# Optimization experiments

Measured on AMD Instinct MI355X. Metric: run time of the kernel, lower is better.

Reference implementation:

```python
import jax, jax.numpy as jnp
import numpy as np

NUM_HEADS, HEAD_SIZE = 8, 80
C = NUM_HEADS * HEAD_SIZE  # 640
GROUPS = 32
EPS = 1e-5


def group_norm(x, gamma, beta):
    b, h, w, c = x.shape
    xg = x.reshape(b, h, w, GROUPS, c // GROUPS)
    mean = xg.mean(axis=(1, 2, 4), keepdims=True)
    var = xg.var(axis=(1, 2, 4), keepdims=True)
    xg = (xg - mean) * jax.lax.rsqrt(var + EPS)
    return xg.reshape(b, h, w, c) * gamma + beta


def layer_norm(x, gamma, beta):
    mean = x.mean(axis=-1, keepdims=True)
    var = x.var(axis=-1, keepdims=True)
    return (x - mean) * jax.lax.rsqrt(var + EPS) * gamma + beta


def cross_attention(x, ctx, wq, wk, wv, wo, bo):
    # x: [B,S,C], ctx: [B,T,Cc]
    b, s, _ = x.shape
    t = ctx.shape[1]
    q = (x @ wq).reshape(b, s, NUM_HEADS, HEAD_SIZE)
    k = (ctx @ wk).reshape(b, t, NUM_HEADS, HEAD_SIZE)
    v = (ctx @ wv).reshape(b, t, NUM_HEADS, HEAD_SIZE)
    scale = HEAD_SIZE ** -0.5
    score = jnp.einsum('bqnh,bknh->bnqk', q, k) * scale
    weights = jax.nn.softmax(score, axis=-1)
    attn = jnp.einsum('bnqk,bknh->bqnh', weights, v)
    return attn.reshape(b, s, C) @ wo + bo


def geglu(x, w, b):
    p = x @ w + b
    xh, gate = p[..., :2560], p[..., 2560:]
    tanh_res = jnp.tanh(gate * 0.7978845608 * (1.0 + 0.044715 * gate * gate))
    return xh * 0.5 * gate * (1.0 + tanh_res)


def setup_inputs() -> dict:
    key = jax.random.key(0)
    ks = iter(jax.random.split(key, 32))
    rn = lambda shape, s=0.02: jax.random.normal(next(ks), shape, dtype=jnp.float32) * s
    inp = {
        'x': jax.random.normal(next(ks), (8, 32, 32, 640), dtype=jnp.float32),
        'context': jax.random.normal(next(ks), (8, 77, 768), dtype=jnp.float32),
        'gn_gamma': jnp.ones((640,), jnp.float32), 'gn_beta': jnp.zeros((640,), jnp.float32),
        'proj_in_w': rn((640, 640)), 'proj_in_b': jnp.zeros((640,), jnp.float32),
        'ln1_g': jnp.ones((640,), jnp.float32), 'ln1_b': jnp.zeros((640,), jnp.float32),
        'a1_q': rn((640, 640)), 'a1_k': rn((640, 640)), 'a1_v': rn((640, 640)),
        'a1_o': rn((640, 640)), 'a1_ob': jnp.zeros((640,), jnp.float32),
        'ln2_g': jnp.ones((640,), jnp.float32), 'ln2_b': jnp.zeros((640,), jnp.float32),
        'a2_q': rn((640, 640)), 'a2_k': rn((768, 640)), 'a2_v': rn((768, 640)),
        'a2_o': rn((640, 640)), 'a2_ob': jnp.zeros((640,), jnp.float32),
        'ln3_g': jnp.ones((640,), jnp.float32), 'ln3_b': jnp.zeros((640,), jnp.float32),
        'ff1_w': rn((640, 5120)), 'ff1_b': jnp.zeros((5120,), jnp.float32),
        'ff2_w': rn((2560, 640)), 'ff2_b': jnp.zeros((640,), jnp.float32),
        'proj_out_w': rn((640, 640)), 'proj_out_b': jnp.zeros((640,), jnp.float32),
    }
    return inp


def reference(x, context, gn_gamma, gn_beta, proj_in_w, proj_in_b,
              ln1_g, ln1_b, a1_q, a1_k, a1_v, a1_o, a1_ob,
              ln2_g, ln2_b, a2_q, a2_k, a2_v, a2_o, a2_ob,
              ln3_g, ln3_b, ff1_w, ff1_b, ff2_w, ff2_b,
              proj_out_w, proj_out_b):
    b, h, w, c = x.shape
    # GroupNorm + 1x1 conv proj_in (== dense over channels)
    y = group_norm(x, gn_gamma, gn_beta)
    y = y @ proj_in_w + proj_in_b
    y = y.reshape(b, h * w, c)
    # Transformer block
    t = cross_attention(layer_norm(y, ln1_g, ln1_b), layer_norm(y, ln1_g, ln1_b), a1_q, a1_k, a1_v, a1_o, a1_ob) + y
    t = cross_attention(layer_norm(t, ln2_g, ln2_b), context, a2_q, a2_k, a2_v, a2_o, a2_ob) + t
    t = geglu(layer_norm(t, ln3_g, ln3_b), ff1_w, ff1_b) @ ff2_w + ff2_b + t
    # proj_out (1x1 conv) + residual
    t = t.reshape(b, h, w, c)
    return t @ proj_out_w + proj_out_b + x
```

## Files before the change

kernel.cpp:

```cpp
#include <hip/hip_runtime.h>
#include <hip/hip_bf16.h>
#include <math.h>

typedef unsigned short u16;
typedef unsigned int u32;
typedef __attribute__((ext_vector_type(8))) short bf16x8;
typedef __attribute__((ext_vector_type(4))) float f32x4;

__device__ __forceinline__ u16 f2b(float f) {
    union { float f; unsigned u; } v; v.f = f;
    unsigned r = v.u + 0x7fffu + ((v.u >> 16) & 1u);
    return (u16)(r >> 16);
}
__device__ __forceinline__ float b2f(u16 h) {
    union { unsigned u; float f; } v; v.u = ((unsigned)h) << 16; return v.f;
}

__device__ __forceinline__ void gld16(const u16* gp, u16* lp) {
    auto g = (const __attribute__((address_space(1))) u32*)gp;
    auto l = (__attribute__((address_space(3))) u32*)lp;
    __builtin_amdgcn_global_load_lds(g, l, 16, 0, 0);
}

__device__ __forceinline__ int swz8(int row, int lb) { return (lb + (row >> 1)) & 7; }

struct GemmP {
    const u16* A; const float* Af; const u16* B;
    const float* bias; const float* res;
    float* Cf; u16* Cb;
    int M, N, K, lda, ldb, ldc;
    float alpha;
};

template<int MT>
__global__ __launch_bounds__(256) void gemm_bt(GemmP p) {
    constexpr int MI = MT / 32;
    __shared__ u16 As[MT * 64];
    __shared__ u16 Bs[128 * 64];
    const int tid = threadIdx.x;
    const int m0 = blockIdx.y * MT, n0 = blockIdx.x * 128;
    const int lane = tid & 63, wave = tid >> 6;
    const int quad = lane >> 4, l16 = lane & 15;
    const int wr = (wave >> 1) * (MT / 2), wc = (wave & 1) * 64;
    const int srow = lane >> 3, pb8 = lane & 7;

    f32x4 acc[MI][4];
#pragma unroll
    for (int i = 0; i < MI; i++)
#pragma unroll
        for (int j = 0; j < 4; j++) acc[i][j] = (f32x4){0.f, 0.f, 0.f, 0.f};

    for (int k0 = 0; k0 < p.K; k0 += 64) {
        if (p.Af) {
            constexpr int TPR = 256 / MT;
            constexpr int NB = 8 / TPR;
            int row = tid / TPR, part = tid % TPR;
            const float* srcr = p.Af + (long)(m0 + row) * p.lda + k0;
#pragma unroll
            for (int q2 = 0; q2 < NB; q2++) {
                int lb = part * NB + q2;
                float4 f0 = *(const float4*)(srcr + lb * 8);
                float4 f1 = *(const float4*)(srcr + lb * 8 + 4);
                u16 tmp[8];
                tmp[0]=f2b(f0.x); tmp[1]=f2b(f0.y); tmp[2]=f2b(f0.z); tmp[3]=f2b(f0.w);
                tmp[4]=f2b(f1.x); tmp[5]=f2b(f1.y); tmp[6]=f2b(f1.z); tmp[7]=f2b(f1.w);
                *(uint4*)&As[row * 64 + swz8(row, lb) * 8] = *(uint4*)tmp;
            }
        } else {
#pragma unroll
            for (int j = 0; j < MT / 32; j++) {
                int rbase = wave * (MT / 4) + j * 8;
                int r = rbase + srow;
                int lb = (pb8 - (r >> 1)) & 7;
                gld16(p.A + (long)(m0 + r) * p.lda + k0 + lb * 8, &As[rbase * 64]);
            }
        }
#pragma unroll
        for (int j = 0; j < 4; j++) {
            int rbase = wave * 32 + j * 8;
            int r = rbase + srow;
            int lb = (pb8 - (r >> 1)) & 7;
            gld16(p.B + (long)(n0 + r) * p.ldb + k0 + lb * 8, &Bs[rbase * 64]);
        }
        __syncthreads();

#pragma unroll
        for (int kk = 0; kk < 2; kk++) {
            bf16x8 af[MI], bfr[4];
#pragma unroll
            for (int mi = 0; mi < MI; mi++) {
                int row = wr + mi * 16 + l16;
                af[mi] = *(const bf16x8*)&As[row * 64 + swz8(row, kk * 4 + quad) * 8];
            }
#pragma unroll
            for (int ni = 0; ni < 4; ni++) {
                int row = wc + ni * 16 + l16;
                bfr[ni] = *(const bf16x8*)&Bs[row * 64 + swz8(row, kk * 4 + quad) * 8];
            }
#pragma unroll
            for (int mi = 0; mi < MI; mi++)
#pragma unroll
                for (int ni = 0; ni < 4; ni++)
                    acc[mi][ni] = __builtin_amdgcn_mfma_f32_16x16x32_bf16(af[mi], bfr[ni], acc[mi][ni], 0, 0, 0);
        }
        __syncthreads();
    }

#pragma unroll
    for (int mi = 0; mi < MI; mi++) {
#pragma unroll
        for (int ni = 0; ni < 4; ni++) {
#pragma unroll
            for (int r = 0; r < 4; r++) {
                int row = m0 + wr + mi * 16 + quad * 4 + r;
                int col = n0 + wc + ni * 16 + l16;
                if (row < p.M && col < p.N) {
                    float v = acc[mi][ni][r] * p.alpha;
                    if (p.bias) v += p.bias[col];
                    long idx = (long)row * p.ldc + col;
                    if (p.res) v += p.res[idx];
                    if (p.Cf) p.Cf[idx] = v; else p.Cb[idx] = f2b(v);
                }
            }
        }
    }
}

struct GegluP {
    const u16* A; const u16* Bx; const u16* Bg;
    const float* bx; const float* bg;
    u16* H;
    int K, lda, ldb, ldh;
};

__global__ __launch_bounds__(256) void gemm_geglu(GegluP p) {
    __shared__ u16 As[128 * 64];
    __shared__ u16 Bxs[128 * 64];
    __shared__ u16 Bgs[128 * 64];
    const int tid = threadIdx.x;
    const int m0 = blockIdx.y * 128, n0 = blockIdx.x * 128;
    const int lane = tid & 63, wave = tid >> 6;
    const int quad = lane >> 4, l16 = lane & 15;
    const int wr = (wave >> 1) * 64, wc = (wave & 1) * 64;
    const int srow = lane >> 3, pb8 = lane & 7;

    f32x4 ax[4][4], ag[4][4];
#pragma unroll
    for (int i = 0; i < 4; i++)
#pragma unroll
        for (int j = 0; j < 4; j++) { ax[i][j] = (f32x4){0.f,0.f,0.f,0.f}; ag[i][j] = (f32x4){0.f,0.f,0.f,0.f}; }

    for (int k0 = 0; k0 < p.K; k0 += 64) {
#pragma unroll
        for (int j = 0; j < 4; j++) {
            int rbase = wave * 32 + j * 8;
            int r = rbase + srow;
            int lb = (pb8 - (r >> 1)) & 7;
            gld16(p.A  + (long)(m0 + r) * p.lda + k0 + lb * 8, &As[rbase * 64]);
            gld16(p.Bx + (long)(n0 + r) * p.ldb + k0 + lb * 8, &Bxs[rbase * 64]);
            gld16(p.Bg + (long)(n0 + r) * p.ldb + k0 + lb * 8, &Bgs[rbase * 64]);
        }
        __syncthreads();

#pragma unroll
        for (int kk = 0; kk < 2; kk++) {
            bf16x8 af[4], bxf[4], bgf[4];
#pragma unroll
            for (int mi = 0; mi < 4; mi++) {
                int row = wr + mi * 16 + l16;
                af[mi] = *(const bf16x8*)&As[row * 64 + swz8(row, kk * 4 + quad) * 8];
            }
#pragma unroll
            for (int ni = 0; ni < 4; ni++) {
                int row = wc + ni * 16 + l16;
                bxf[ni] = *(const bf16x8*)&Bxs[row * 64 + swz8(row, kk * 4 + quad) * 8];
                bgf[ni] = *(const bf16x8*)&Bgs[row * 64 + swz8(row, kk * 4 + quad) * 8];
            }
#pragma unroll
            for (int mi = 0; mi < 4; mi++)
#pragma unroll
                for (int ni = 0; ni < 4; ni++) {
                    ax[mi][ni] = __builtin_amdgcn_mfma_f32_16x16x32_bf16(af[mi], bxf[ni], ax[mi][ni], 0, 0, 0);
                    ag[mi][ni] = __builtin_amdgcn_mfma_f32_16x16x32_bf16(af[mi], bgf[ni], ag[mi][ni], 0, 0, 0);
                }
        }
        __syncthreads();
    }

#pragma unroll
    for (int mi = 0; mi < 4; mi++) {
#pragma unroll
        for (int ni = 0; ni < 4; ni++) {
#pragma unroll
            for (int r = 0; r < 4; r++) {
                int row = m0 + wr + mi * 16 + quad * 4 + r;
                int col = wc + ni * 16 + l16;
                float xh = ax[mi][ni][r] + p.bx[n0 + col];
                float g  = ag[mi][ni][r] + p.bg[n0 + col];
                float u  = 0.7978845608f * g * (1.0f + 0.044715f * g * g);
                float s  = 1.0f / (1.0f + __expf(-2.0f * u));
                p.H[(long)row * p.ldh + n0 + col] = f2b(xh * g * s);
            }
        }
    }
}

struct FlashP {
    const u16* Q; const u16* K; const u16* V;
    u16* O;
    int ldq, ldk, ldv, ldo;
    int S, TS, nIter;
    long qBatch, kBatch;
    float scale;
};

__global__ __launch_bounds__(256, 2) void flash_attn(FlashP p) {
    __shared__ u16 shU[128 * 136];
    __shared__ u16 shV[80 * 136];
    const int z = blockIdx.x, b = z >> 3, h = z & 7;
    const int q0 = blockIdx.z * 128;
    const int tid = threadIdx.x, lane = tid & 63, w = tid >> 6;
    const int quad = lane >> 4, l16 = lane & 15;

    const u16* Qp = p.Q + (long)b * p.qBatch + (long)q0 * p.ldq + h * 80;
    const u16* Kp = p.K + (long)b * p.kBatch + h * 80;
    const u16* Vp = p.V + (long)b * p.kBatch + h * 80;

    for (int idx = tid; idx < 128 * 12; idx += 256) {
        int row = idx / 12, g = idx - row * 12;
        uint4 v = {0, 0, 0, 0};
        if (g < 10) v = *(const uint4*)(Qp + (long)row * p.ldq + g * 8);
        *(uint4*)&shU[row * 104 + g * 8] = v;
    }
    __syncthreads();
    bf16x8 qf[2][3];
#pragma unroll
    for (int mi = 0; mi < 2; mi++)
#pragma unroll
        for (int kk = 0; kk < 3; kk++)
            qf[mi][kk] = *(const bf16x8*)&shU[(w * 32 + mi * 16 + l16) * 104 + kk * 32 + quad * 8];
    __syncthreads();

    float m_[2][4], l_[2][4];
    f32x4 acc_o[2][5];
#pragma unroll
    for (int mi = 0; mi < 2; mi++) {
#pragma unroll
        for (int r = 0; r < 4; r++) { m_[mi][r] = -1e30f; l_[mi][r] = 0.f; }
#pragma unroll
        for (int ni = 0; ni < 5; ni++) acc_o[mi][ni] = (f32x4){0.f, 0.f, 0.f, 0.f};
    }

    for (int it = 0; it < p.nIter; it++) {
        const int s0 = it * 128;
        for (int idx = tid; idx < 128 * 12; idx += 256) {
            int row = idx / 12, g = idx - row * 12;
            uint4 v = {0, 0, 0, 0};
            if (g < 10 && (s0 + row) < p.TS)
                v = *(const uint4*)(Kp + (long)(s0 + row) * p.ldk + g * 8);
            *(uint4*)&shU[row * 104 + g * 8] = v;
        }
        for (int idx = tid; idx < 128 * 10; idx += 256) {
            int row = idx / 10, g = idx - row * 10;
            uint4 v = {0, 0, 0, 0};
            if ((s0 + row) < p.TS)
                v = *(const uint4*)(Vp + (long)(s0 + row) * p.ldv + g * 8);
            u16 tmp[8]; *(uint4*)tmp = v;
#pragma unroll
            for (int j = 0; j < 8; j++) shV[(g * 8 + j) * 136 + row] = tmp[j];
        }
        __syncthreads();

        f32x4 acc_s[2][8];
#pragma unroll
        for (int mi = 0; mi < 2; mi++)
#pragma unroll
            for (int ni = 0; ni < 8; ni++) acc_s[mi][ni] = (f32x4){0.f, 0.f, 0.f, 0.f};
#pragma unroll
        for (int kk = 0; kk < 3; kk++) {
            bf16x8 kf[8];
#pragma unroll
            for (int ni = 0; ni < 8; ni++)
                kf[ni] = *(const bf16x8*)&shU[(ni * 16 + l16) * 104 + kk * 32 + quad * 8];
#pragma unroll
            for (int mi = 0; mi < 2; mi++)
#pragma unroll
                for (int ni = 0; ni < 8; ni++)
                    acc_s[mi][ni] = __builtin_amdgcn_mfma_f32_16x16x32_bf16(qf[mi][kk], kf[ni], acc_s[mi][ni], 0, 0, 0);
        }
        __syncthreads();

#pragma unroll
        for (int mi = 0; mi < 2; mi++) {
#pragma unroll
            for (int ni = 0; ni < 8; ni++) {
                bool valid = (s0 + ni * 16 + l16) < p.TS;
#pragma unroll
                for (int r = 0; r < 4; r++)
                    acc_s[mi][ni][r] = valid ? acc_s[mi][ni][r] * p.scale : -1e30f;
            }
#pragma unroll
            for (int r = 0; r < 4; r++) {
                float rm = acc_s[mi][0][r];
#pragma unroll
                for (int ni = 1; ni < 8; ni++) rm = fmaxf(rm, acc_s[mi][ni][r]);
#pragma unroll
                for (int msk = 1; msk < 16; msk <<= 1) rm = fmaxf(rm, __shfl_xor(rm, msk));
                float mn = fmaxf(m_[mi][r], rm);
                float al = __expf(m_[mi][r] - mn);
                m_[mi][r] = mn;
                float rs = 0.f;
                int prow = (w * 32 + mi * 16 + quad * 4 + r) * 136;
#pragma unroll
                for (int ni = 0; ni < 8; ni++) {
                    float pv = __expf(acc_s[mi][ni][r] - mn);
                    rs += pv;
                    shU[prow + ni * 16 + l16] = f2b(pv);
                }
#pragma unroll
                for (int msk = 1; msk < 16; msk <<= 1) rs += __shfl_xor(rs, msk);
                l_[mi][r] = l_[mi][r] * al + rs;
#pragma unroll
                for (int ni = 0; ni < 5; ni++) acc_o[mi][ni][r] *= al;
            }
        }
        __syncthreads();

#pragma unroll
        for (int kk = 0; kk < 4; kk++) {
            bf16x8 vf[5], pf[2];
#pragma unroll
            for (int ni = 0; ni < 5; ni++)
                vf[ni] = *(const bf16x8*)&shV[(ni * 16 + l16) * 136 + kk * 32 + quad * 8];
#pragma unroll
            for (int mi = 0; mi < 2; mi++)
                pf[mi] = *(const bf16x8*)&shU[(w * 32 + mi * 16 + l16) * 136 + kk * 32 + quad * 8];
#pragma unroll
            for (int mi = 0; mi < 2; mi++)
#pragma unroll
                for (int ni = 0; ni < 5; ni++)
                    acc_o[mi][ni] = __builtin_amdgcn_mfma_f32_16x16x32_bf16(pf[mi], vf[ni], acc_o[mi][ni], 0, 0, 0);
        }
        __syncthreads();
    }

    u16* Op = p.O + ((long)b * p.S + q0) * p.ldo + h * 80;
#pragma unroll
    for (int mi = 0; mi < 2; mi++) {
#pragma unroll
        for (int r = 0; r < 4; r++) {
            float inv = 1.0f / l_[mi][r];
            int row = w * 32 + mi * 16 + quad * 4 + r;
#pragma unroll
            for (int ni = 0; ni < 5; ni++)
                Op[(long)row * p.ldo + ni * 16 + l16] = f2b(acc_o[mi][ni][r] * inv);
        }
    }
}

struct WT8 { const float* W[8]; u16* Wt[8]; };

__global__ void wtrans8(WT8 p, int K, int N) {
    __shared__ float tile[32][33];
    const float* W = p.W[blockIdx.z];
    u16* Wt = p.Wt[blockIdx.z];
    int n0 = blockIdx.x * 32, k0 = blockIdx.y * 32;
    int tx = threadIdx.x, ty = threadIdx.y;
#pragma unroll
    for (int i = 0; i < 4; i++) {
        int k = k0 + ty + i * 8, n = n0 + tx;
        if (k < K && n < N) tile[ty + i * 8][tx] = W[(long)k * N + n];
    }
    __syncthreads();
#pragma unroll
    for (int i = 0; i < 4; i++) {
        int n = n0 + ty + i * 8, k = k0 + tx;
        if (n < N && k < K) Wt[(long)n * K + k] = f2b(tile[tx][ty + i * 8]);
    }
}

__global__ void gn_stats(const float* __restrict__ x, float* __restrict__ stats) {
    int bid = blockIdx.x;
    int b = bid >> 5, g = bid & 31;
    const float* base = x + (long)b * 32 * 32 * 640 + g * 20;
    float s = 0.f, sq = 0.f;
    for (int idx = threadIdx.x; idx < 32 * 32 * 20; idx += 256) {
        int hw = idx / 20, c = idx - hw * 20;
        float v = base[(long)hw * 640 + c];
        s += v; sq += v * v;
    }
    __shared__ float rs[256], rq[256];
    rs[threadIdx.x] = s; rq[threadIdx.x] = sq; __syncthreads();
    for (int t = 128; t > 0; t >>= 1) {
        if (threadIdx.x < t) { rs[threadIdx.x] += rs[threadIdx.x + t]; rq[threadIdx.x] += rq[threadIdx.x + t]; }
        __syncthreads();
    }
    if (threadIdx.x == 0) {
        float mean = rs[0] / 20480.0f;
        float var = rq[0] / 20480.0f - mean * mean;
        stats[bid * 2] = mean;
        stats[bid * 2 + 1] = rsqrtf(var + 1e-5f);
    }
}

__global__ void gn_apply(const float* __restrict__ x, const float* __restrict__ stats,
                         const float* __restrict__ gamma, const float* __restrict__ beta,
                         u16* __restrict__ out) {
    long i = (long)blockIdx.x * 256 + threadIdx.x;
    int c = (int)(i % 640);
    int b = (int)(i / (32 * 32 * 640));
    int g = c / 20;
    float mean = stats[(b * 32 + g) * 2], inv = stats[(b * 32 + g) * 2 + 1];
    out[i] = f2b((x[i] - mean) * inv * gamma[c] + beta[c]);
}

__global__ void layernorm_rows(const float* __restrict__ X, const float* __restrict__ g,
                               const float* __restrict__ be, u16* __restrict__ out, int nrows) {
    int row = blockIdx.x * 4 + (threadIdx.x >> 6);
    int lane = threadIdx.x & 63;
    if (row >= nrows) return;
    const float* x = X + (long)row * 640;
    float v[10];
    float s = 0.f;
#pragma unroll
    for (int i = 0; i < 10; i++) { v[i] = x[lane + i * 64]; s += v[i]; }
#pragma unroll
    for (int m = 1; m < 64; m <<= 1) s += __shfl_xor(s, m);
    float mean = s * (1.0f / 640.0f);
    float sq = 0.f;
#pragma unroll
    for (int i = 0; i < 10; i++) { float d = v[i] - mean; sq += d * d; }
#pragma unroll
    for (int m = 1; m < 64; m <<= 1) sq += __shfl_xor(sq, m);
    float inv = rsqrtf(sq * (1.0f / 640.0f) + 1e-5f);
    u16* o = out + (long)row * 640;
#pragma unroll
    for (int i = 0; i < 10; i++) {
        int c = lane + i * 64;
        o[c] = f2b((v[i] - mean) * inv * g[c] + be[c]);
    }
}

__global__ void f2b_k(const float* __restrict__ src, u16* __restrict__ dst, long n) {
    long i = (long)blockIdx.x * 256 + threadIdx.x;
    if (i < n) dst[i] = f2b(src[i]);
}

extern "C" void kernel_launch(void* const* d_in, const int* in_sizes, int n_in,
                              void* d_out, int out_size, void* d_ws, size_t ws_size,
                              hipStream_t stream) {
    const float* x        = (const float*)d_in[0];
    const float* context  = (const float*)d_in[1];
    const float* gn_gamma = (const float*)d_in[2];
    const float* gn_beta  = (const float*)d_in[3];
    const float* proj_in_w = (const float*)d_in[4];
    const float* proj_in_b = (const float*)d_in[5];
    const float* ln1_g = (const float*)d_in[6];
    const float* ln1_b = (const float*)d_in[7];
    const float* a1_q = (const float*)d_in[8];
    const float* a1_k = (const float*)d_in[9];
    const float* a1_v = (const float*)d_in[10];
    const float* a1_o = (const float*)d_in[11];
    const float* a1_ob = (const float*)d_in[12];
    const float* ln2_g = (const float*)d_in[13];
    const float* ln2_b = (const float*)d_in[14];
    const float* a2_q = (const float*)d_in[15];
    const float* a2_k = (const float*)d_in[16];
    const float* a2_v = (const float*)d_in[17];
    const float* a2_o = (const float*)d_in[18];
    const float* a2_ob = (const float*)d_in[19];
    const float* ln3_g = (const float*)d_in[20];
    const float* ln3_b = (const float*)d_in[21];
    const float* ff1_w = (const float*)d_in[22];
    const float* ff1_b = (const float*)d_in[23];
    const float* ff2_w = (const float*)d_in[24];
    const float* ff2_b = (const float*)d_in[25];
    const float* proj_out_w = (const float*)d_in[26];
    const float* proj_out_b = (const float*)d_in[27];
    float* out = (float*)d_out;

    char* ws = (char*)d_ws;
    size_t off = 0;
    auto alloc = [&](size_t bytes) -> void* {
        void* p = ws + off;
        off += (bytes + 255) & ~(size_t)255;
        return p;
    };
    u16* Wt_pi  = (u16*)alloc(640 * 640 * 2);
    u16* Wt_qkv = (u16*)alloc((size_t)1920 * 640 * 2);
    u16* Wt_1o  = (u16*)alloc(640 * 640 * 2);
    u16* Wt_2q  = (u16*)alloc(640 * 640 * 2);
    u16* Wt_kv2 = (u16*)alloc((size_t)1280 * 768 * 2);
    u16* Wt_2o  = (u16*)alloc(640 * 640 * 2);
    u16* Wt_f1  = (u16*)alloc((size_t)5120 * 640 * 2);
    u16* Wt_f2  = (u16*)alloc((size_t)640 * 2560 * 2);
    u16* Wt_po  = (u16*)alloc(640 * 640 * 2);
    float* t    = (float*)alloc((size_t)8192 * 640 * 4);
    u16* bufA   = (u16*)alloc((size_t)8192 * 640 * 2);
    u16* big    = (u16*)alloc((size_t)8192 * 2560 * 2);
    u16* kv2b   = (u16*)alloc((size_t)616 * 1280 * 2);
    u16* ctxb   = (u16*)alloc((size_t)616 * 768 * 2);
    float* stats = (float*)alloc(256 * 2 * 4);
    (void)alloc(65536);
    u16* qkvb = big;
    u16* hb   = big;

    const float SCALE = 0.11180339887498949f;

    auto gemm1 = [&](const u16* A, const float* Af, const u16* Bt, const float* bias,
                     const float* res, float* Cf, u16* Cb, int M, int N, int K,
                     int lda, int ldb, int ldc, float alpha, int mt) {
        GemmP p{};
        p.A = A; p.Af = Af; p.B = Bt; p.bias = bias; p.res = res; p.Cf = Cf; p.Cb = Cb;
        p.M = M; p.N = N; p.K = K; p.lda = lda; p.ldb = ldb; p.ldc = ldc;
        p.alpha = alpha;
        dim3 grid((N + 127) / 128, (M + mt - 1) / mt, 1);
        if (mt == 64) gemm_bt<64><<<grid, 256, 0, stream>>>(p);
        else          gemm_bt<128><<<grid, 256, 0, stream>>>(p);
    };

    {
        dim3 blk(32, 8);
        WT8 sq{};
        sq.W[0] = proj_in_w; sq.Wt[0] = Wt_pi;
        sq.W[1] = a1_q;      sq.Wt[1] = Wt_qkv;
        sq.W[2] = a1_k;      sq.Wt[2] = Wt_qkv + 640 * 640;
        sq.W[3] = a1_v;      sq.Wt[3] = Wt_qkv + 2 * 640 * 640;
        sq.W[4] = a1_o;      sq.Wt[4] = Wt_1o;
        sq.W[5] = a2_q;      sq.Wt[5] = Wt_2q;
        sq.W[6] = a2_o;      sq.Wt[6] = Wt_2o;
        sq.W[7] = proj_out_w; sq.Wt[7] = Wt_po;
        wtrans8<<<dim3(20, 20, 8), blk, 0, stream>>>(sq, 640, 640);
        WT8 kv{};
        kv.W[0] = a2_k; kv.Wt[0] = Wt_kv2;
        kv.W[1] = a2_v; kv.Wt[1] = Wt_kv2 + (size_t)640 * 768;
        wtrans8<<<dim3(20, 24, 2), blk, 0, stream>>>(kv, 768, 640);
        WT8 f1{}; f1.W[0] = ff1_w; f1.Wt[0] = Wt_f1;
        wtrans8<<<dim3(160, 20, 1), blk, 0, stream>>>(f1, 640, 5120);
        WT8 f2{}; f2.W[0] = ff2_w; f2.Wt[0] = Wt_f2;
        wtrans8<<<dim3(20, 80, 1), blk, 0, stream>>>(f2, 2560, 640);
    }

    gn_stats<<<256, 256, 0, stream>>>(x, stats);
    gn_apply<<<20480, 256, 0, stream>>>(x, stats, gn_gamma, gn_beta, bufA);
    gemm1(bufA, nullptr, Wt_pi, proj_in_b, nullptr, t, nullptr, 8192, 640, 640, 640, 640, 640, 1.0f, 64);

    layernorm_rows<<<2048, 256, 0, stream>>>(t, ln1_g, ln1_b, bufA, 8192);
    gemm1(bufA, nullptr, Wt_qkv, nullptr, nullptr, nullptr, qkvb, 8192, 1920, 640, 640, 640, 1920, 1.0f, 128);
    {
        FlashP p{};
        p.Q = qkvb; p.K = qkvb + 640; p.V = qkvb + 1280; p.O = bufA;
        p.ldq = 1920; p.ldk = 1920; p.ldv = 1920; p.ldo = 640;
        p.S = 1024; p.TS = 1024; p.nIter = 8;
        p.qBatch = (long)1024 * 1920; p.kBatch = (long)1024 * 1920;
        p.scale = SCALE;
        flash_attn<<<dim3(64, 1, 8), 256, 0, stream>>>(p);
    }
    gemm1(bufA, nullptr, Wt_1o, a1_ob, t, t, nullptr, 8192, 640, 640, 640, 640, 640, 1.0f, 64);

    layernorm_rows<<<2048, 256, 0, stream>>>(t, ln2_g, ln2_b, bufA, 8192);
    f2b_k<<<1848, 256, 0, stream>>>(context, ctxb, 473088);
    gemm1(bufA, nullptr, Wt_2q, nullptr, nullptr, nullptr, qkvb, 8192, 640, 640, 640, 640, 640, 1.0f, 64);
    gemm1(ctxb, nullptr, Wt_kv2, nullptr, nullptr, nullptr, kv2b, 616, 1280, 768, 768, 768, 1280, 1.0f, 64);
    {
        FlashP p{};
        p.Q = qkvb; p.K = kv2b; p.V = kv2b + 640; p.O = bufA;
        p.ldq = 640; p.ldk = 1280; p.ldv = 1280; p.ldo = 640;
        p.S = 1024; p.TS = 77; p.nIter = 1;
        p.qBatch = (long)1024 * 640; p.kBatch = (long)77 * 1280;
        p.scale = SCALE;
        flash_attn<<<dim3(64, 1, 8), 256, 0, stream>>>(p);
    }
    gemm1(bufA, nullptr, Wt_2o, a2_ob, t, t, nullptr, 8192, 640, 640, 640, 640, 640, 1.0f, 64);

    layernorm_rows<<<2048, 256, 0, stream>>>(t, ln3_g, ln3_b, bufA, 8192);
    {
        GegluP p{};
        p.A = bufA; p.Bx = Wt_f1; p.Bg = Wt_f1 + (size_t)2560 * 640;
        p.bx = ff1_b; p.bg = ff1_b + 2560;
        p.H = hb;
        p.K = 640; p.lda = 640; p.ldb = 640; p.ldh = 2560;
        gemm_geglu<<<dim3(20, 64), 256, 0, stream>>>(p);
    }
    gemm1(hb, nullptr, Wt_f2, ff2_b, t, t, nullptr, 8192, 640, 2560, 2560, 2560, 640, 1.0f, 64);

    gemm1(nullptr, t, Wt_po, proj_out_b, x, out, nullptr, 8192, 640, 640, 640, 640, 640, 1.0f, 64);
}
```

Baseline: 699.7 us.

## Double-buffer LDS in GEMM kernels and drop fp32-A load path

```diff
diff --git a/kernel.cpp b/kernel.cpp
--- a/kernel.cpp
+++ b/kernel.cpp
@@ -22,10 +22,10 @@
     __builtin_amdgcn_global_load_lds(g, l, 16, 0, 0);
 }
 
-__device__ __forceinline__ int swz8(int row, int lb) { return (lb + (row >> 1)) & 7; }
+__device__ __forceinline__ int swz4(int row, int q) { return (q + (row >> 1)) & 3; }
 
 struct GemmP {
-    const u16* A; const float* Af; const u16* B;
+    const u16* A; const u16* B;
     const float* bias; const float* res;
     float* Cf; u16* Cb;
     int M, N, K, lda, ldb, ldc;
@@ -35,14 +35,14 @@
 template<int MT>
 __global__ __launch_bounds__(256) void gemm_bt(GemmP p) {
     constexpr int MI = MT / 32;
-    __shared__ u16 As[MT * 64];
-    __shared__ u16 Bs[128 * 64];
+    __shared__ u16 As[2][MT * 64];
+    __shared__ u16 Bs[2][128 * 64];
     const int tid = threadIdx.x;
     const int m0 = blockIdx.y * MT, n0 = blockIdx.x * 128;
     const int lane = tid & 63, wave = tid >> 6;
     const int quad = lane >> 4, l16 = lane & 15;
     const int wr = (wave >> 1) * (MT / 2), wc = (wave & 1) * 64;
-    const int srow = lane >> 3, pb8 = lane & 7;
+    const int srow4 = lane >> 2, pcb4 = lane & 3;
 
     f32x4 acc[MI][4];
 #pragma unroll
@@ -50,52 +50,45 @@
 #pragma unroll
         for (int j = 0; j < 4; j++) acc[i][j] = (f32x4){0.f, 0.f, 0.f, 0.f};
 
-    for (int k0 = 0; k0 < p.K; k0 += 64) {
-        if (p.Af) {
-            constexpr int TPR = 256 / MT;
-            constexpr int NB = 8 / TPR;
-            int row = tid / TPR, part = tid % TPR;
-            const float* srcr = p.Af + (long)(m0 + row) * p.lda + k0;
-#pragma unroll
-            for (int q2 = 0; q2 < NB; q2++) {
-                int lb = part * NB + q2;
-                float4 f0 = *(const float4*)(srcr + lb * 8);
-                float4 f1 = *(const float4*)(srcr + lb * 8 + 4);
-                u16 tmp[8];
-                tmp[0]=f2b(f0.x); tmp[1]=f2b(f0.y); tmp[2]=f2b(f0.z); tmp[3]=f2b(f0.w);
-                tmp[4]=f2b(f1.x); tmp[5]=f2b(f1.y); tmp[6]=f2b(f1.z); tmp[7]=f2b(f1.w);
-                *(uint4*)&As[row * 64 + swz8(row, lb) * 8] = *(uint4*)tmp;
-            }
-        } else {
-#pragma unroll
-            for (int j = 0; j < MT / 32; j++) {
-                int rbase = wave * (MT / 4) + j * 8;
-                int r = rbase + srow;
-                int lb = (pb8 - (r >> 1)) & 7;
-                gld16(p.A + (long)(m0 + r) * p.lda + k0 + lb * 8, &As[rbase * 64]);
-            }
-        }
-#pragma unroll
-        for (int j = 0; j < 4; j++) {
-            int rbase = wave * 32 + j * 8;
-            int r = rbase + srow;
-            int lb = (pb8 - (r >> 1)) & 7;
-            gld16(p.B + (long)(n0 + r) * p.ldb + k0 + lb * 8, &Bs[rbase * 64]);
-        }
-        __syncthreads();
-
-#pragma unroll
-        for (int kk = 0; kk < 2; kk++) {
+    auto stage = [&](int buf, int k0) {
+#pragma unroll
+        for (int c = 0; c < MT / 32; c++) {
+            int cc = wave * (MT / 32) + c;
+            int sub = cc / (MT / 16), rg = cc % (MT / 16);
+            int r = rg * 16 + srow4;
+            int lcb = (pcb4 - (r >> 1)) & 3;
+            gld16(p.A + (long)(m0 + r) * p.lda + k0 + sub * 32 + lcb * 8,
+                  &As[buf][sub * (MT * 32) + rg * 512]);
+        }
+#pragma unroll
+        for (int c = 0; c < 4; c++) {
+            int cc = wave * 4 + c;
+            int sub = cc >> 3, rg = cc & 7;
+            int r = rg * 16 + srow4;
+            int lcb = (pcb4 - (r >> 1)) & 3;
+            gld16(p.B + (long)(n0 + r) * p.ldb + k0 + sub * 32 + lcb * 8,
+                  &Bs[buf][sub * 4096 + rg * 512]);
+        }
+    };
+
+    const int nIter = p.K >> 6;
+    stage(0, 0);
+    int buf = 0;
+    for (int it = 0; it < nIter; it++) {
+        __syncthreads();
+        if (it + 1 < nIter) stage(buf ^ 1, (it + 1) << 6);
+#pragma unroll
+        for (int sub = 0; sub < 2; sub++) {
             bf16x8 af[MI], bfr[4];
 #pragma unroll
             for (int mi = 0; mi < MI; mi++) {
                 int row = wr + mi * 16 + l16;
-                af[mi] = *(const bf16x8*)&As[row * 64 + swz8(row, kk * 4 + quad) * 8];
+                af[mi] = *(const bf16x8*)&As[buf][sub * (MT * 32) + row * 32 + swz4(row, quad) * 8];
             }
 #pragma unroll
             for (int ni = 0; ni < 4; ni++) {
                 int row = wc + ni * 16 + l16;
-                bfr[ni] = *(const bf16x8*)&Bs[row * 64 + swz8(row, kk * 4 + quad) * 8];
+                bfr[ni] = *(const bf16x8*)&Bs[buf][sub * 4096 + row * 32 + swz4(row, quad) * 8];
             }
 #pragma unroll
             for (int mi = 0; mi < MI; mi++)
@@ -103,7 +96,7 @@
                 for (int ni = 0; ni < 4; ni++)
                     acc[mi][ni] = __builtin_amdgcn_mfma_f32_16x16x32_bf16(af[mi], bfr[ni], acc[mi][ni], 0, 0, 0);
         }
-        __syncthreads();
+        buf ^= 1;
     }
 
 #pragma unroll
@@ -134,15 +127,15 @@
 };
 
 __global__ __launch_bounds__(256) void gemm_geglu(GegluP p) {
-    __shared__ u16 As[128 * 64];
-    __shared__ u16 Bxs[128 * 64];
-    __shared__ u16 Bgs[128 * 64];
+    __shared__ u16 As[2][128 * 32];
+    __shared__ u16 Bxs[2][128 * 32];
+    __shared__ u16 Bgs[2][128 * 32];
     const int tid = threadIdx.x;
     const int m0 = blockIdx.y * 128, n0 = blockIdx.x * 128;
     const int lane = tid & 63, wave = tid >> 6;
     const int quad = lane >> 4, l16 = lane & 15;
     const int wr = (wave >> 1) * 64, wc = (wave & 1) * 64;
-    const int srow = lane >> 3, pb8 = lane & 7;
+    const int srow4 = lane >> 2, pcb4 = lane & 3;
 
     f32x4 ax[4][4], ag[4][4];
 #pragma unroll
@@ -150,41 +143,44 @@
 #pragma unroll
         for (int j = 0; j < 4; j++) { ax[i][j] = (f32x4){0.f,0.f,0.f,0.f}; ag[i][j] = (f32x4){0.f,0.f,0.f,0.f}; }
 
-    for (int k0 = 0; k0 < p.K; k0 += 64) {
-#pragma unroll
-        for (int j = 0; j < 4; j++) {
-            int rbase = wave * 32 + j * 8;
-            int r = rbase + srow;
-            int lb = (pb8 - (r >> 1)) & 7;
-            gld16(p.A  + (long)(m0 + r) * p.lda + k0 + lb * 8, &As[rbase * 64]);
-            gld16(p.Bx + (long)(n0 + r) * p.ldb + k0 + lb * 8, &Bxs[rbase * 64]);
-            gld16(p.Bg + (long)(n0 + r) * p.ldb + k0 + lb * 8, &Bgs[rbase * 64]);
-        }
-        __syncthreads();
-
-#pragma unroll
-        for (int kk = 0; kk < 2; kk++) {
-            bf16x8 af[4], bxf[4], bgf[4];
-#pragma unroll
-            for (int mi = 0; mi < 4; mi++) {
-                int row = wr + mi * 16 + l16;
-                af[mi] = *(const bf16x8*)&As[row * 64 + swz8(row, kk * 4 + quad) * 8];
-            }
+    auto stage = [&](int buf, int k0) {
+#pragma unroll
+        for (int c = 0; c < 2; c++) {
+            int rg = wave * 2 + c;
+            int r = rg * 16 + srow4;
+            int lcb = (pcb4 - (r >> 1)) & 3;
+            gld16(p.A  + (long)(m0 + r) * p.lda + k0 + lcb * 8, &As[buf][rg * 512]);
+            gld16(p.Bx + (long)(n0 + r) * p.ldb + k0 + lcb * 8, &Bxs[buf][rg * 512]);
+            gld16(p.Bg + (long)(n0 + r) * p.ldb + k0 + lcb * 8, &Bgs[buf][rg * 512]);
+        }
+    };
+
+    const int nIter = p.K >> 5;
+    stage(0, 0);
+    int buf = 0;
+    for (int it = 0; it < nIter; it++) {
+        __syncthreads();
+        if (it + 1 < nIter) stage(buf ^ 1, (it + 1) << 5);
+        bf16x8 af[4], bxf[4], bgf[4];
+#pragma unroll
+        for (int mi = 0; mi < 4; mi++) {
+            int row = wr + mi * 16 + l16;
+            af[mi] = *(const bf16x8*)&As[buf][row * 32 + swz4(row, quad) * 8];
+        }
+#pragma unroll
+        for (int ni = 0; ni < 4; ni++) {
+            int row = wc + ni * 16 + l16;
+            bxf[ni] = *(const bf16x8*)&Bxs[buf][row * 32 + swz4(row, quad) * 8];
+            bgf[ni] = *(const bf16x8*)&Bgs[buf][row * 32 + swz4(row, quad) * 8];
+        }
+#pragma unroll
+        for (int mi = 0; mi < 4; mi++)
 #pragma unroll
             for (int ni = 0; ni < 4; ni++) {
-                int row = wc + ni * 16 + l16;
-                bxf[ni] = *(const bf16x8*)&Bxs[row * 64 + swz8(row, kk * 4 + quad) * 8];
-                bgf[ni] = *(const bf16x8*)&Bgs[row * 64 + swz8(row, kk * 4 + quad) * 8];
-            }
-#pragma unroll
-            for (int mi = 0; mi < 4; mi++)
-#pragma unroll
-                for (int ni = 0; ni < 4; ni++) {
-                    ax[mi][ni] = __builtin_amdgcn_mfma_f32_16x16x32_bf16(af[mi], bxf[ni], ax[mi][ni], 0, 0, 0);
-                    ag[mi][ni] = __builtin_amdgcn_mfma_f32_16x16x32_bf16(af[mi], bgf[ni], ag[mi][ni], 0, 0, 0);
-                }
-        }
-        __syncthreads();
+                ax[mi][ni] = __builtin_amdgcn_mfma_f32_16x16x32_bf16(af[mi], bxf[ni], ax[mi][ni], 0, 0, 0);
+                ag[mi][ni] = __builtin_amdgcn_mfma_f32_16x16x32_bf16(af[mi], bgf[ni], ag[mi][ni], 0, 0, 0);
+            }
+        buf ^= 1;
     }
 
 #pragma unroll
@@ -501,17 +497,17 @@
     u16* kv2b   = (u16*)alloc((size_t)616 * 1280 * 2);
     u16* ctxb   = (u16*)alloc((size_t)616 * 768 * 2);
     float* stats = (float*)alloc(256 * 2 * 4);
-    (void)alloc(65536);
+    (void)alloc(131072);
     u16* qkvb = big;
     u16* hb   = big;
 
     const float SCALE = 0.11180339887498949f;
 
-    auto gemm1 = [&](const u16* A, const float* Af, const u16* Bt, const float* bias,
+    auto gemm1 = [&](const u16* A, const u16* Bt, const float* bias,
                      const float* res, float* Cf, u16* Cb, int M, int N, int K,
                      int lda, int ldb, int ldc, float alpha, int mt) {
         GemmP p{};
-        p.A = A; p.Af = Af; p.B = Bt; p.bias = bias; p.res = res; p.Cf = Cf; p.Cb = Cb;
+        p.A = A; p.B = Bt; p.bias = bias; p.res = res; p.Cf = Cf; p.Cb = Cb;
         p.M = M; p.N = N; p.K = K; p.lda = lda; p.ldb = ldb; p.ldc = ldc;
         p.alpha = alpha;
         dim3 grid((N + 127) / 128, (M + mt - 1) / mt, 1);
@@ -543,10 +539,10 @@
 
     gn_stats<<<256, 256, 0, stream>>>(x, stats);
     gn_apply<<<20480, 256, 0, stream>>>(x, stats, gn_gamma, gn_beta, bufA);
-    gemm1(bufA, nullptr, Wt_pi, proj_in_b, nullptr, t, nullptr, 8192, 640, 640, 640, 640, 640, 1.0f, 64);
+    gemm1(bufA, Wt_pi, proj_in_b, nullptr, t, nullptr, 8192, 640, 640, 640, 640, 640, 1.0f, 64);
 
     layernorm_rows<<<2048, 256, 0, stream>>>(t, ln1_g, ln1_b, bufA, 8192);
-    gemm1(bufA, nullptr, Wt_qkv, nullptr, nullptr, nullptr, qkvb, 8192, 1920, 640, 640, 640, 1920, 1.0f, 128);
+    gemm1(bufA, Wt_qkv, nullptr, nullptr, nullptr, qkvb, 8192, 1920, 640, 640, 640, 1920, 1.0f, 64);
     {
         FlashP p{};
         p.Q = qkvb; p.K = qkvb + 640; p.V = qkvb + 1280; p.O = bufA;
@@ -556,12 +552,12 @@
         p.scale = SCALE;
         flash_attn<<<dim3(64, 1, 8), 256, 0, stream>>>(p);
     }
-    gemm1(bufA, nullptr, Wt_1o, a1_ob, t, t, nullptr, 8192, 640, 640, 640, 640, 640, 1.0f, 64);
+    gemm1(bufA, Wt_1o, a1_ob, t, t, nullptr, 8192, 640, 640, 640, 640, 640, 1.0f, 64);
 
     layernorm_rows<<<2048, 256, 0, stream>>>(t, ln2_g, ln2_b, bufA, 8192);
     f2b_k<<<1848, 256, 0, stream>>>(context, ctxb, 473088);
-    gemm1(bufA, nullptr, Wt_2q, nullptr, nullptr, nullptr, qkvb, 8192, 640, 640, 640, 640, 640, 1.0f, 64);
-    gemm1(ctxb, nullptr, Wt_kv2, nullptr, nullptr, nullptr, kv2b, 616, 1280, 768, 768, 768, 1280, 1.0f, 64);
+    gemm1(bufA, Wt_2q, nullptr, nullptr, nullptr, qkvb, 8192, 640, 640, 640, 640, 640, 1.0f, 64);
+    gemm1(ctxb, Wt_kv2, nullptr, nullptr, nullptr, kv2b, 616, 1280, 768, 768, 768, 1280, 1.0f, 64);
     {
         FlashP p{};
         p.Q = qkvb; p.K = kv2b; p.V = kv2b + 640; p.O = bufA;
@@ -571,7 +567,7 @@
         p.scale = SCALE;
         flash_attn<<<dim3(64, 1, 8), 256, 0, stream>>>(p);
     }
-    gemm1(bufA, nullptr, Wt_2o, a2_ob, t, t, nullptr, 8192, 640, 640, 640, 640, 640, 1.0f, 64);
+    gemm1(bufA, Wt_2o, a2_ob, t, t, nullptr, 8192, 640, 640, 640, 640, 640, 1.0f, 64);
 
     layernorm_rows<<<2048, 256, 0, stream>>>(t, ln3_g, ln3_b, bufA, 8192);
     {
@@ -582,7 +578,8 @@
         p.K = 640; p.lda = 640; p.ldb = 640; p.ldh = 2560;
         gemm_geglu<<<dim3(20, 64), 256, 0, stream>>>(p);
     }
-    gemm1(hb, nullptr, Wt_f2, ff2_b, t, t, nullptr, 8192, 640, 2560, 2560, 2560, 640, 1.0f, 64);
-
-    gemm1(nullptr, t, Wt_po, proj_out_b, x, out, nullptr, 8192, 640, 640, 640, 640, 640, 1.0f, 64);
-}
+    gemm1(hb, Wt_f2, ff2_b, t, t, nullptr, 8192, 640, 2560, 2560, 2560, 640, 1.0f, 64);
+
+    f2b_k<<<20480, 256, 0, stream>>>(t, bufA, 5242880);
+    gemm1(bufA, Wt_po, proj_out_b, x, out, nullptr, 8192, 640, 640, 640, 640, 640, 1.0f, 64);
+}
```

After: 710.7 us. No clear change (+1.6%).
